# Optimization experiments

Hardware: AMD Instinct MI355X
Metric: run time of the kernel (lower is better)

Reference implementation:

```python
import jax, jax.numpy as jnp
import numpy as np

GAMMA1 = 4.0

def setup_inputs() -> dict:
    key = jax.random.key(0)
    k1, k2 = jax.random.split(key)
    image_feature = jax.random.normal(k1, (128, 17, 17, 1024), dtype=jnp.float32)
    word_vector = jax.random.normal(k2, (128, 32, 1024), dtype=jnp.float32)
    return {"image_feature": image_feature, "word_vector": word_vector}

def reference(image_feature, word_vector):
    B, H, W, D = image_feature.shape
    T = word_vector.shape[1]
    # context: [B, HW, D]
    context = image_feature.reshape(B, H * W, D)
    # attn scores: [B, HW, T] = context @ word_vector^T
    attn = jnp.einsum('bnd,btd->bnt', context, word_vector)
    # first softmax over words (last dim of [B*HW, T])
    attn = jax.nn.softmax(attn, axis=-1)
    # transpose to [B, T, HW], scale by gamma1, softmax over regions
    attn = jnp.transpose(attn, (0, 2, 1))
    attn = jax.nn.softmax(GAMMA1 * attn, axis=-1)
    # region_context: [B, D, T] = context^T @ attn^T
    region_context = jnp.einsum('bnd,btn->bdt', context, attn)
    return region_context
```

## Files before the change

kernel.cpp:

```cpp
#include <hip/hip_runtime.h>

#define NB 128
#define NN 289
#define ND 1024
#define NT 32
#define GAMMA1 4.0f

typedef __attribute__((ext_vector_type(4))) float f32x4;
typedef __attribute__((ext_vector_type(8))) short bf8;

__device__ inline void split2(float x, ushort &h, ushort &l) {
    uint u = __float_as_uint(x);
    h = (ushort)(u >> 16);
    float hf = __uint_as_float(u & 0xFFFF0000u);
    l = (ushort)(__float_as_uint(x - hf) >> 16);
}
__device__ inline uint packhl(float x) {
    uint u = __float_as_uint(x);
    float hf = __uint_as_float(u & 0xFFFF0000u);
    uint lo = __float_as_uint(x - hf) >> 16;
    return (u & 0xFFFF0000u) | lo;
}
__device__ inline void unpack8(const uint *u, bf8 &hi, bf8 &lo) {
    union { uint w[4]; bf8 v; } H, L;
#pragma unroll
    for (int k = 0; k < 4; ++k) {
        H.w[k] = (u[2 * k] >> 16) | (u[2 * k + 1] & 0xFFFF0000u);
        L.w[k] = (u[2 * k] & 0xFFFFu) | (u[2 * k + 1] << 16);
    }
    hi = H.v; lo = L.v;
}

__global__ __launch_bounds__(128) void damsm_attn_a(
    const float* __restrict__ img, const float* __restrict__ word,
    float* __restrict__ E)
{
    __shared__ ushort sAh[32][72], sAl[32][72];
    __shared__ ushort sBh[32][72], sBl[32][72];

    const int bid = blockIdx.x;
    const int xcd = bid & 7;
    const int s   = bid >> 3;
    const int b   = xcd * 16 + s / 10;
    const int m   = s % 10;
    const int n0  = m * 32;

    const int tid = threadIdx.x;
    const int w   = tid >> 6;
    const int l   = tid & 63;
    const int lr  = l & 15;
    const int lh  = l >> 4;

    const float* __restrict__ imgb  = img  + (size_t)b * NN * ND;
    const float* __restrict__ wordb = word + (size_t)b * NT * ND;

    f32x4 acc[2];
#pragma unroll
    for (int ct = 0; ct < 2; ++ct) acc[ct] = (f32x4){0.f, 0.f, 0.f, 0.f};

    for (int kc = 0; kc < 16; ++kc) {
#pragma unroll
        for (int it = 0; it < 4; ++it) {
            int idx = tid + 128 * it;
            int row = idx >> 4;
            int q   = idx & 15;
            int n   = n0 + row;
            float4 v = make_float4(0.f, 0.f, 0.f, 0.f);
            if (n < NN)
                v = *(const float4*)(imgb + (size_t)n * ND + kc * 64 + q * 4);
            union { ushort us[4]; uint2 u2; } H, L;
            split2(v.x, H.us[0], L.us[0]); split2(v.y, H.us[1], L.us[1]);
            split2(v.z, H.us[2], L.us[2]); split2(v.w, H.us[3], L.us[3]);
            *(uint2*)(&sAh[row][q * 4]) = H.u2;
            *(uint2*)(&sAl[row][q * 4]) = L.u2;
        }
#pragma unroll
        for (int it = 0; it < 4; ++it) {
            int idx = tid + 128 * it;
            int row = idx >> 4;
            int q   = idx & 15;
            float4 v = *(const float4*)(wordb + (size_t)row * ND + kc * 64 + q * 4);
            union { ushort us[4]; uint2 u2; } H, L;
            split2(v.x, H.us[0], L.us[0]); split2(v.y, H.us[1], L.us[1]);
            split2(v.z, H.us[2], L.us[2]); split2(v.w, H.us[3], L.us[3]);
            *(uint2*)(&sBh[row][q * 4]) = H.u2;
            *(uint2*)(&sBl[row][q * 4]) = L.u2;
        }
        __syncthreads();

#pragma unroll
        for (int ks = 0; ks < 2; ++ks) {
            const int ko = ks * 32 + 8 * lh;
            bf8 ah = *(const bf8*)(&sAh[16 * w + lr][ko]);
            bf8 al = *(const bf8*)(&sAl[16 * w + lr][ko]);
#pragma unroll
            for (int ct = 0; ct < 2; ++ct) {
                bf8 bh = *(const bf8*)(&sBh[16 * ct + lr][ko]);
                bf8 bl = *(const bf8*)(&sBl[16 * ct + lr][ko]);
                acc[ct] = __builtin_amdgcn_mfma_f32_16x16x32_bf16(ah, bh, acc[ct], 0, 0, 0);
                acc[ct] = __builtin_amdgcn_mfma_f32_16x16x32_bf16(ah, bl, acc[ct], 0, 0, 0);
                acc[ct] = __builtin_amdgcn_mfma_f32_16x16x32_bf16(al, bh, acc[ct], 0, 0, 0);
            }
        }
        __syncthreads();
    }

#pragma unroll
    for (int r = 0; r < 4; ++r) {
        float v0 = acc[0][r], v1 = acc[1][r];
        float mx = fmaxf(v0, v1);
#pragma unroll
        for (int sh = 1; sh < 16; sh <<= 1) mx = fmaxf(mx, __shfl_xor(mx, sh));
        float e0 = __expf(v0 - mx), e1 = __expf(v1 - mx);
        float ss = e0 + e1;
#pragma unroll
        for (int sh = 1; sh < 16; sh <<= 1) ss += __shfl_xor(ss, sh);
        float inv = 1.0f / ss;
        float E0 = __expf(GAMMA1 * (e0 * inv));
        float E1 = __expf(GAMMA1 * (e1 * inv));
        int n = n0 + 16 * w + 4 * lh + r;
        if (n < NN) {
            float* dst = E + ((size_t)b * NN + n) * NT;
            dst[lr]      = E0;
            dst[lr + 16] = E1;
        }
    }
}

__global__ __launch_bounds__(256) void damsm_attn_b(
    const float* __restrict__ img, const float* __restrict__ E,
    float* __restrict__ out)
{
    __shared__ uint  sEt[32 * 321];
    __shared__ uint  sCt[128 * 33];
    __shared__ float sOut[128 * 36];
    __shared__ float sCs[NT];

    const int bid = blockIdx.x;
    const int b   = bid >> 3;
    const int d0  = (bid & 7) * 128;

    const int tid = threadIdx.x;
    const int w   = tid >> 6;
    const int l   = tid & 63;
    const int lr  = l & 15;
    const int lh  = l >> 4;

    const float* __restrict__ Eb   = E   + (size_t)b * NN * NT;
    const float* __restrict__ imgb = img + (size_t)b * NN * ND;

    if (tid < NT) sCs[tid] = 0.f;
    __syncthreads();

    for (int idx = tid; idx < (NN * NT) / 4; idx += 256) {
        int n  = idx >> 3;
        int tq = idx & 7;
        float4 v = *(const float4*)(Eb + (size_t)idx * 4);
        sEt[(tq * 4 + 0) * 321 + n] = packhl(v.x);
        sEt[(tq * 4 + 1) * 321 + n] = packhl(v.y);
        sEt[(tq * 4 + 2) * 321 + n] = packhl(v.z);
        sEt[(tq * 4 + 3) * 321 + n] = packhl(v.w);
        atomicAdd(&sCs[tq * 4 + 0], v.x);
        atomicAdd(&sCs[tq * 4 + 1], v.y);
        atomicAdd(&sCs[tq * 4 + 2], v.z);
        atomicAdd(&sCs[tq * 4 + 3], v.w);
    }
    for (int idx = tid; idx < 32 * 32; idx += 256) {
        int t = idx >> 5;
        int n = NN + (idx & 31);
        sEt[t * 321 + n] = 0u;
    }
    __syncthreads();
    if (tid < NT) sCs[tid] = 1.0f / sCs[tid];
    __syncthreads();

    f32x4 acc[2][2];
#pragma unroll
    for (int rt = 0; rt < 2; ++rt)
#pragma unroll
        for (int ct = 0; ct < 2; ++ct) acc[rt][ct] = (f32x4){0.f, 0.f, 0.f, 0.f};

    for (int kc = 0; kc < 10; ++kc) {
        const int nc0 = kc * 32;
#pragma unroll
        for (int it = 0; it < 4; ++it) {
            int idx = tid + 256 * it;
            int nn  = idx >> 5;
            int q   = idx & 31;
            int n   = nc0 + nn;
            float4 v = make_float4(0.f, 0.f, 0.f, 0.f);
            if (n < NN)
                v = *(const float4*)(imgb + (size_t)n * ND + d0 + q * 4);
            sCt[(q * 4 + 0) * 33 + nn] = packhl(v.x);
            sCt[(q * 4 + 1) * 33 + nn] = packhl(v.y);
            sCt[(q * 4 + 2) * 33 + nn] = packhl(v.z);
            sCt[(q * 4 + 3) * 33 + nn] = packhl(v.w);
        }
        __syncthreads();

        uint ua[8];
        bf8 ahi[2], alo[2];
#pragma unroll
        for (int rt = 0; rt < 2; ++rt) {
            int base = (16 * rt + lr) * 321 + nc0 + 8 * lh;
#pragma unroll
            for (int e = 0; e < 8; ++e) ua[e] = sEt[base + e];
            unpack8(ua, ahi[rt], alo[rt]);
        }
#pragma unroll
        for (int ct = 0; ct < 2; ++ct) {
            int base = (32 * w + 16 * ct + lr) * 33 + 8 * lh;
            uint ub[8];
#pragma unroll
            for (int e = 0; e < 8; ++e) ub[e] = sCt[base + e];
            bf8 bhi, blo;
            unpack8(ub, bhi, blo);
#pragma unroll
            for (int rt = 0; rt < 2; ++rt) {
                acc[rt][ct] = __builtin_amdgcn_mfma_f32_16x16x32_bf16(ahi[rt], bhi, acc[rt][ct], 0, 0, 0);
                acc[rt][ct] = __builtin_amdgcn_mfma_f32_16x16x32_bf16(ahi[rt], blo, acc[rt][ct], 0, 0, 0);
                acc[rt][ct] = __builtin_amdgcn_mfma_f32_16x16x32_bf16(alo[rt], bhi, acc[rt][ct], 0, 0, 0);
            }
        }
        __syncthreads();
    }

#pragma unroll
    for (int rt = 0; rt < 2; ++rt)
#pragma unroll
        for (int ct = 0; ct < 2; ++ct) {
            int dl = 32 * w + 16 * ct + lr;
#pragma unroll
            for (int r = 0; r < 4; ++r) {
                int t = 16 * rt + 4 * lh + r;
                sOut[dl * 36 + t] = acc[rt][ct][r] * sCs[t];
            }
        }
    __syncthreads();

    float* __restrict__ outb = out + (size_t)b * ND * NT;
#pragma unroll
    for (int it = 0; it < 4; ++it) {
        int idx = tid + 256 * it;
        int dl  = idx >> 3;
        int tq  = idx & 7;
        float4 v = *(const float4*)(&sOut[dl * 36 + tq * 4]);
        *(float4*)(outb + (size_t)(d0 + dl) * NT + tq * 4) = v;
    }
}

extern "C" void kernel_launch(void* const* d_in, const int* in_sizes, int n_in,
                              void* d_out, int out_size, void* d_ws, size_t ws_size,
                              hipStream_t stream) {
    const float* img  = (const float*)d_in[0];
    const float* word = (const float*)d_in[1];
    float* out = (float*)d_out;
    float* E   = (float*)d_ws;

    hipLaunchKernelGGL(damsm_attn_a, dim3(1280), dim3(128), 0, stream, img, word, E);
    hipLaunchKernelGGL(damsm_attn_b, dim3(1024), dim3(256), 0, stream, img, E, out);
}
```

Baseline: 335.6 us.

## Replace split-bf16 MFMA in second GEMM with fp32 FMA and precomputed column sums

Kernel A now reduces the per-word exp sums with shuffles and global atomics into a workspace buffer, which is zeroed by a memset before launch. Kernel B no longer transposes and splits E and the context into hi/lo bf16 pairs for three MFMAs per tile. Instead it does a plain fp32 FMA outer-product GEMM over shared-memory tiles with a 4x4 register block per thread. This removes the packing, atomic and transpose overhead in B and keeps full fp32 precision, but gives up the matrix cores and adds a memset plus global atomics.

```diff
diff --git a/kernel.cpp b/kernel.cpp
--- a/kernel.cpp
+++ b/kernel.cpp
@@ -15,25 +15,10 @@
     float hf = __uint_as_float(u & 0xFFFF0000u);
     l = (ushort)(__float_as_uint(x - hf) >> 16);
 }
-__device__ inline uint packhl(float x) {
-    uint u = __float_as_uint(x);
-    float hf = __uint_as_float(u & 0xFFFF0000u);
-    uint lo = __float_as_uint(x - hf) >> 16;
-    return (u & 0xFFFF0000u) | lo;
-}
-__device__ inline void unpack8(const uint *u, bf8 &hi, bf8 &lo) {
-    union { uint w[4]; bf8 v; } H, L;
-#pragma unroll
-    for (int k = 0; k < 4; ++k) {
-        H.w[k] = (u[2 * k] >> 16) | (u[2 * k + 1] & 0xFFFF0000u);
-        L.w[k] = (u[2 * k] & 0xFFFFu) | (u[2 * k + 1] << 16);
-    }
-    hi = H.v; lo = L.v;
-}
 
 __global__ __launch_bounds__(128) void damsm_attn_a(
     const float* __restrict__ img, const float* __restrict__ word,
-    float* __restrict__ E)
+    float* __restrict__ E, float* __restrict__ csum)
 {
     __shared__ ushort sAh[32][72], sAl[32][72];
     __shared__ ushort sBh[32][72], sBl[32][72];
@@ -105,6 +90,7 @@
         __syncthreads();
     }
 
+    float cs0 = 0.f, cs1 = 0.f;
 #pragma unroll
     for (int r = 0; r < 4; ++r) {
         float v0 = acc[0][r], v1 = acc[1][r];
@@ -123,129 +109,111 @@
             float* dst = E + ((size_t)b * NN + n) * NT;
             dst[lr]      = E0;
             dst[lr + 16] = E1;
-        }
+            cs0 += E0;
+            cs1 += E1;
+        }
+    }
+    cs0 += __shfl_xor(cs0, 16); cs0 += __shfl_xor(cs0, 32);
+    cs1 += __shfl_xor(cs1, 16); cs1 += __shfl_xor(cs1, 32);
+    if (lh == 0) {
+        atomicAdd(&csum[b * NT + lr], cs0);
+        atomicAdd(&csum[b * NT + lr + 16], cs1);
     }
 }
 
 __global__ __launch_bounds__(256) void damsm_attn_b(
     const float* __restrict__ img, const float* __restrict__ E,
-    float* __restrict__ out)
+    const float* __restrict__ csum, float* __restrict__ out)
 {
-    __shared__ uint  sEt[32 * 321];
-    __shared__ uint  sCt[128 * 33];
-    __shared__ float sOut[128 * 36];
-    __shared__ float sCs[NT];
-
-    const int bid = blockIdx.x;
-    const int b   = bid >> 3;
-    const int d0  = (bid & 7) * 128;
-
+    __shared__ float s_E[NN][NT];
+    __shared__ float s_ctx[24][128];
+
+    const int b   = blockIdx.y;
+    const int d0  = blockIdx.x * 128;
     const int tid = threadIdx.x;
-    const int w   = tid >> 6;
-    const int l   = tid & 63;
-    const int lr  = l & 15;
-    const int lh  = l >> 4;
+    const int p   = tid >> 3;
+    const int q   = tid & 7;
 
     const float* __restrict__ Eb   = E   + (size_t)b * NN * NT;
     const float* __restrict__ imgb = img + (size_t)b * NN * ND;
 
-    if (tid < NT) sCs[tid] = 0.f;
+    for (int idx = tid; idx < (NN * NT) / 4; idx += 256)
+        ((float4*)s_E)[idx] = ((const float4*)Eb)[idx];
+
+    float4 cs = *(const float4*)(csum + b * NT + q * 4);
+    float4 ci;
+    ci.x = 1.0f / cs.x; ci.y = 1.0f / cs.y; ci.z = 1.0f / cs.z; ci.w = 1.0f / cs.w;
     __syncthreads();
 
-    for (int idx = tid; idx < (NN * NT) / 4; idx += 256) {
-        int n  = idx >> 3;
-        int tq = idx & 7;
-        float4 v = *(const float4*)(Eb + (size_t)idx * 4);
-        sEt[(tq * 4 + 0) * 321 + n] = packhl(v.x);
-        sEt[(tq * 4 + 1) * 321 + n] = packhl(v.y);
-        sEt[(tq * 4 + 2) * 321 + n] = packhl(v.z);
-        sEt[(tq * 4 + 3) * 321 + n] = packhl(v.w);
-        atomicAdd(&sCs[tq * 4 + 0], v.x);
-        atomicAdd(&sCs[tq * 4 + 1], v.y);
-        atomicAdd(&sCs[tq * 4 + 2], v.z);
-        atomicAdd(&sCs[tq * 4 + 3], v.w);
-    }
-    for (int idx = tid; idx < 32 * 32; idx += 256) {
-        int t = idx >> 5;
-        int n = NN + (idx & 31);
-        sEt[t * 321 + n] = 0u;
-    }
-    __syncthreads();
-    if (tid < NT) sCs[tid] = 1.0f / sCs[tid];
-    __syncthreads();
-
-    f32x4 acc[2][2];
-#pragma unroll
-    for (int rt = 0; rt < 2; ++rt)
-#pragma unroll
-        for (int ct = 0; ct < 2; ++ct) acc[rt][ct] = (f32x4){0.f, 0.f, 0.f, 0.f};
-
-    for (int kc = 0; kc < 10; ++kc) {
-        const int nc0 = kc * 32;
-#pragma unroll
-        for (int it = 0; it < 4; ++it) {
+    float acc[4][4];
+#pragma unroll
+    for (int a = 0; a < 4; ++a)
+#pragma unroll
+        for (int c = 0; c < 4; ++c) acc[a][c] = 0.f;
+
+    for (int nc = 0; nc < 288; nc += 24) {
+#pragma unroll
+        for (int it = 0; it < 3; ++it) {
             int idx = tid + 256 * it;
-            int nn  = idx >> 5;
-            int q   = idx & 31;
-            int n   = nc0 + nn;
-            float4 v = make_float4(0.f, 0.f, 0.f, 0.f);
-            if (n < NN)
-                v = *(const float4*)(imgb + (size_t)n * ND + d0 + q * 4);
-            sCt[(q * 4 + 0) * 33 + nn] = packhl(v.x);
-            sCt[(q * 4 + 1) * 33 + nn] = packhl(v.y);
-            sCt[(q * 4 + 2) * 33 + nn] = packhl(v.z);
-            sCt[(q * 4 + 3) * 33 + nn] = packhl(v.w);
-        }
-        __syncthreads();
-
-        uint ua[8];
-        bf8 ahi[2], alo[2];
-#pragma unroll
-        for (int rt = 0; rt < 2; ++rt) {
-            int base = (16 * rt + lr) * 321 + nc0 + 8 * lh;
-#pragma unroll
-            for (int e = 0; e < 8; ++e) ua[e] = sEt[base + e];
-            unpack8(ua, ahi[rt], alo[rt]);
-        }
-#pragma unroll
-        for (int ct = 0; ct < 2; ++ct) {
-            int base = (32 * w + 16 * ct + lr) * 33 + 8 * lh;
-            uint ub[8];
-#pragma unroll
-            for (int e = 0; e < 8; ++e) ub[e] = sCt[base + e];
-            bf8 bhi, blo;
-            unpack8(ub, bhi, blo);
-#pragma unroll
-            for (int rt = 0; rt < 2; ++rt) {
-                acc[rt][ct] = __builtin_amdgcn_mfma_f32_16x16x32_bf16(ahi[rt], bhi, acc[rt][ct], 0, 0, 0);
-                acc[rt][ct] = __builtin_amdgcn_mfma_f32_16x16x32_bf16(ahi[rt], blo, acc[rt][ct], 0, 0, 0);
-                acc[rt][ct] = __builtin_amdgcn_mfma_f32_16x16x32_bf16(alo[rt], bhi, acc[rt][ct], 0, 0, 0);
-            }
-        }
-        __syncthreads();
-    }
-
-#pragma unroll
-    for (int rt = 0; rt < 2; ++rt)
-#pragma unroll
-        for (int ct = 0; ct < 2; ++ct) {
-            int dl = 32 * w + 16 * ct + lr;
-#pragma unroll
-            for (int r = 0; r < 4; ++r) {
-                int t = 16 * rt + 4 * lh + r;
-                sOut[dl * 36 + t] = acc[rt][ct][r] * sCs[t];
-            }
-        }
-    __syncthreads();
-
-    float* __restrict__ outb = out + (size_t)b * ND * NT;
-#pragma unroll
-    for (int it = 0; it < 4; ++it) {
-        int idx = tid + 256 * it;
-        int dl  = idx >> 3;
-        int tq  = idx & 7;
-        float4 v = *(const float4*)(&sOut[dl * 36 + tq * 4]);
-        *(float4*)(outb + (size_t)(d0 + dl) * NT + tq * 4) = v;
+            int nl  = idx >> 5;
+            int dq  = idx & 31;
+            *(float4*)(&s_ctx[nl][dq * 4]) =
+                *(const float4*)(imgb + (size_t)(nc + nl) * ND + d0 + dq * 4);
+        }
+        __syncthreads();
+#pragma unroll 4
+        for (int nn = 0; nn < 24; ++nn) {
+            float4 c = *(const float4*)(&s_ctx[nn][p * 4]);
+            float4 e = *(const float4*)(&s_E[nc + nn][q * 4]);
+            acc[0][0] = fmaf(c.x, e.x, acc[0][0]);
+            acc[0][1] = fmaf(c.x, e.y, acc[0][1]);
+            acc[0][2] = fmaf(c.x, e.z, acc[0][2]);
+            acc[0][3] = fmaf(c.x, e.w, acc[0][3]);
+            acc[1][0] = fmaf(c.y, e.x, acc[1][0]);
+            acc[1][1] = fmaf(c.y, e.y, acc[1][1]);
+            acc[1][2] = fmaf(c.y, e.z, acc[1][2]);
+            acc[1][3] = fmaf(c.y, e.w, acc[1][3]);
+            acc[2][0] = fmaf(c.z, e.x, acc[2][0]);
+            acc[2][1] = fmaf(c.z, e.y, acc[2][1]);
+            acc[2][2] = fmaf(c.z, e.z, acc[2][2]);
+            acc[2][3] = fmaf(c.z, e.w, acc[2][3]);
+            acc[3][0] = fmaf(c.w, e.x, acc[3][0]);
+            acc[3][1] = fmaf(c.w, e.y, acc[3][1]);
+            acc[3][2] = fmaf(c.w, e.z, acc[3][2]);
+            acc[3][3] = fmaf(c.w, e.w, acc[3][3]);
+        }
+        __syncthreads();
+    }
+    {
+        float4 e = *(const float4*)(&s_E[288][q * 4]);
+        float4 c = *(const float4*)(imgb + (size_t)288 * ND + d0 + p * 4);
+        acc[0][0] = fmaf(c.x, e.x, acc[0][0]);
+        acc[0][1] = fmaf(c.x, e.y, acc[0][1]);
+        acc[0][2] = fmaf(c.x, e.z, acc[0][2]);
+        acc[0][3] = fmaf(c.x, e.w, acc[0][3]);
+        acc[1][0] = fmaf(c.y, e.x, acc[1][0]);
+        acc[1][1] = fmaf(c.y, e.y, acc[1][1]);
+        acc[1][2] = fmaf(c.y, e.z, acc[1][2]);
+        acc[1][3] = fmaf(c.y, e.w, acc[1][3]);
+        acc[2][0] = fmaf(c.z, e.x, acc[2][0]);
+        acc[2][1] = fmaf(c.z, e.y, acc[2][1]);
+        acc[2][2] = fmaf(c.z, e.z, acc[2][2]);
+        acc[2][3] = fmaf(c.z, e.w, acc[2][3]);
+        acc[3][0] = fmaf(c.w, e.x, acc[3][0]);
+        acc[3][1] = fmaf(c.w, e.y, acc[3][1]);
+        acc[3][2] = fmaf(c.w, e.z, acc[3][2]);
+        acc[3][3] = fmaf(c.w, e.w, acc[3][3]);
+    }
+
+#pragma unroll
+    for (int di = 0; di < 4; ++di) {
+        int d = d0 + p * 4 + di;
+        float4 v;
+        v.x = acc[di][0] * ci.x;
+        v.y = acc[di][1] * ci.y;
+        v.z = acc[di][2] * ci.z;
+        v.w = acc[di][3] * ci.w;
+        *(float4*)(out + (size_t)(b * ND + d) * NT + q * 4) = v;
     }
 }
 
@@ -254,9 +222,14 @@
                               hipStream_t stream) {
     const float* img  = (const float*)d_in[0];
     const float* word = (const float*)d_in[1];
-    float* out = (float*)d_out;
-    float* E   = (float*)d_ws;
-
-    hipLaunchKernelGGL(damsm_attn_a, dim3(1280), dim3(128), 0, stream, img, word, E);
-    hipLaunchKernelGGL(damsm_attn_b, dim3(1024), dim3(256), 0, stream, img, E, out);
-}
+    float* out  = (float*)d_out;
+    float* csum = (float*)d_ws;
+    float* E    = csum + NB * NT;
+
+    hipMemsetAsync(csum, 0, NB * NT * sizeof(float), stream);
+
+    hipLaunchKernelGGL(damsm_attn_a, dim3(1280), dim3(128), 0, stream,
+                       img, word, E, csum);
+    hipLaunchKernelGGL(damsm_attn_b, dim3(8, 128), dim3(256), 0, stream,
+                       img, E, csum, out);
+}
```

Result: faster. 293.8 us (-12.4%).
